# Kernel tuning notes

Hardware: AMD Instinct MI355X
Metric: run time of the kernel (lower is better)

## Reference

```python
import jax, jax.numpy as jnp
import numpy as np

NALGOS = 64
NTASKS = 256
T = 4096  # len(lx)


def setup_inputs() -> dict:
    key = jax.random.key(0)
    ks = jax.random.split(key, 6)
    return {
        "lx": jax.random.randint(ks[0], (T,), 0, NTASKS),
        # task_matrix ~ U(-1, 1), as in the torch init
        "task_matrix": jax.random.uniform(ks[1], (NTASKS, NTASKS), jnp.float32) * 2.0 - 1.0,
        # task difficulty ~ U(0, 1); keep away from 0 to avoid division blowup
        "task_difficulty": jax.random.uniform(ks[2], (NTASKS,), jnp.float32, 0.05, 1.0),
        "alg_efficiency": 0.5 + 0.02 * jax.random.normal(ks[3], (NALGOS,), jnp.float32),
        "alg_memory_horizon": 0.5 + 0.1 * jax.random.normal(ks[4], (NALGOS,), jnp.float32),
        "alg_experience_boost": 0.5 + 0.02 * jax.random.normal(ks[5], (NALGOS,), jnp.float32),
    }


def reference(lx, task_matrix, task_difficulty, alg_efficiency,
              alg_memory_horizon, alg_experience_boost):
    # Faithful translation of IdealLearner.performance.
    # Original triple loop reads result[algo,task2,ind] and sig[algo,task,ind]
    # (previous timestep only) and writes index ind+1, so each timestep is
    # vectorizable over (algo, task2); only the time axis is a true recurrence.
    A = alg_efficiency.shape[0]
    N = task_matrix.shape[0]
    eff = alg_efficiency[:, None]        # (A,1)
    mem = alg_memory_horizon[:, None]    # (A,1)
    boost = alg_experience_boost[:, None]  # (A,1)
    diff = task_difficulty[None, :]      # (1,N) ; task_difficulty_scale == 1

    def step(carry, task):
        res_prev, sig_prev = carry              # each (A, N)
        tm = task_matrix[task][None, :]         # (1, N) row for current task
        sp = sig_prev[:, task][:, None]         # (A, 1) prior perf on current task
        res = res_prev * mem + tm * eff + tm * sp * boost
        sig = 2.0 * jax.nn.sigmoid(res / diff) - 1.0
        return (res, sig), sig

    z = jnp.zeros((A, N), task_matrix.dtype)
    _, ys = jax.lax.scan(step, (z, z), lx)      # ys: (T, A, N)
    # prepend the zero initial state -> (A, N, T+1), matching the torch output
    return jnp.concatenate([z[:, :, None], jnp.transpose(ys, (1, 2, 0))], axis=-1)
```

## Files before the change

### kernel.cpp

```cpp
#include <hip/hip_runtime.h>
#include <hip/hip_bf16.h>

#define NALGOS 64
#define NTASKS 256
#define TSTEPS 4096
#define CHUNK  256
#define NCHUNK (TSTEPS / CHUNK)
#define SUB    64
#define TP     257
#define LOG2E  1.44269504f

__global__ __launch_bounds__(64) void driver_kernel(
    const int* __restrict__ lx, const float* __restrict__ tmat,
    const float* __restrict__ diff, const float* __restrict__ eff_v,
    const float* __restrict__ mem_v, const float* __restrict__ boost_v,
    float* __restrict__ g_arr, float* __restrict__ ckpt) {
  __shared__ int    lx_s[TSTEPS + 16];
  __shared__ float  c_s[NTASKS];
  __shared__ float4 ctab[TSTEPS + 8];

  const int a = blockIdx.x;
  const int l = threadIdx.x;
  const float eff   = eff_v[a];
  const float mem   = mem_v[a];
  const float boost = boost_v[a];
  const float e0 = eff - boost;
  const float b2 = 2.0f * boost;

#pragma unroll 8
  for (int k = 0; k < TSTEPS / 64; ++k) lx_s[k * 64 + l] = lx[k * 64 + l];
  if (l < 16) lx_s[TSTEPS + l] = 0;
#pragma unroll
  for (int k = 0; k < NTASKS / 64; ++k) {
    float dk = diff[k * 64 + l];
    c_s[k * 64 + l] = -LOG2E / dk;
  }
  __syncthreads();

#pragma unroll 4
  for (int k = 0; k < TSTEPS / 64; ++k) {
    int i  = k * 64 + l;
    int t0 = lx_s[i];
    int t1 = lx_s[i + 1];
    float q  = tmat[t0 * NTASKS + t1];
    float cp = c_s[t1];
    float4 e;
    e.x = cp;
    e.y = b2 * cp * q;
    e.z = e0 * cp * q;
    e.w = __int_as_float(lx_s[i + 2] | (lx_s[i + 8] << 16));
    ctab[i] = e;
  }
  if (l < 8) ctab[TSTEPS + l] = make_float4(0.f, 0.f, 0.f, __int_as_float(0));
  __syncthreads();

  const float4* rows = (const float4*)tmat;
  float* gout = g_arr + (size_t)a * TSTEPS;
  float* ck   = ckpt  + (size_t)a * NCHUNK * NTASKS;

  float r0 = 0.f, r1 = 0.f, r2 = 0.f, r3 = 0.f;
  float u = 2.0f;
  float keep_g = 0.f;

  float4 ctr[4];
  float4 tmr[8];
#pragma unroll
  for (int k = 0; k < 4; ++k) ctr[k] = ctab[k];
#pragma unroll
  for (int k = 0; k < 8; ++k) tmr[k] = rows[lx_s[k] * 64 + l];
  float A = ctr[0].z;

  for (int grp = 0; grp < TSTEPS / 64; ++grp) {
#pragma unroll 1
    for (int k32 = 0; k32 < 2; ++k32) {
      const float4* cb = ctab + grp * 64 + k32 * 32;
      const int kb = k32 * 32;
#pragma unroll
      for (int kk = 0; kk < 32; ++kk) {
        const int k = kb + kk;
        const float4 ct  = ctr[k & 3];
        const float4 ctn = ctr[(k + 1) & 3];
        const float4 tm  = tmr[k & 7];

        float w   = __builtin_amdgcn_rcpf(u);
        float gt  = fmaf(b2, w, e0);
        float arg = fmaf(ct.y, w, A);
        float ev  = __builtin_amdgcn_exp2f(arg);
        u = 1.0f + ev;

        keep_g = (k == l) ? gt : keep_g;

        r0 = fmaf(r0, mem, tm.x * gt);
        r1 = fmaf(r1, mem, tm.y * gt);
        r2 = fmaf(r2, mem, tm.z * gt);
        r3 = fmaf(r3, mem, tm.w * gt);

        const int sw   = __builtin_amdgcn_readfirstlane(__float_as_int(ct.w));
        const int j2   = sw & 0xff;
        const int lane = j2 >> 2;
        float h01  = (j2 & 1) ? r1 : r0;
        float h23  = (j2 & 1) ? r3 : r2;
        float hsel = (j2 & 2) ? h23 : h01;
        float bro = __uint_as_float(
            __builtin_amdgcn_readlane(__float_as_uint(hsel), lane));
        float p = mem * bro;
        A = fmaf(ctn.x, p, ctn.z);

        ctr[k & 3] = cb[kk + 4];
        const int nrow = (sw >> 16) & 0xff;
        tmr[k & 7] = rows[nrow * 64 + l];
      }
    }
    gout[grp * 64 + l] = keep_g;
    if ((grp & 3) == 3 && grp != 63) {
      float4 s; s.x = r0; s.y = r1; s.z = r2; s.w = r3;
      ((float4*)(ck + ((grp + 1) >> 2) * NTASKS))[l] = s;
    }
  }
}

__global__ __launch_bounds__(256) void expand_kernel(
    const int* __restrict__ lx, const float* __restrict__ tmat,
    const float* __restrict__ diff, const float* __restrict__ mem_v,
    const float* __restrict__ g_arr, const float* __restrict__ ckpt,
    float* __restrict__ out) {
  __shared__ float tile[SUB * TP];
  __shared__ int   lx_c[CHUNK];
  __shared__ float g_c[CHUNK];

  const int id = blockIdx.x;
  const int c  = (id >> 3) & 15;
  const int a  = (id & 7) + 8 * (id >> 7);
  const int n  = threadIdx.x;

  const float mem = mem_v[a];
  const float cn  = -LOG2E / diff[n];
  float res = (c == 0) ? 0.f : ckpt[((size_t)a * NCHUNK + c) * NTASKS + n];

  const int t0 = c * CHUNK;
  lx_c[n] = lx[t0 + n];
  g_c[n]  = g_arr[(size_t)a * TSTEPS + t0 + n];
  __syncthreads();

  if (c == 0) out[((size_t)a * NTASKS + n) * (TSTEPS + 1)] = 0.f;

  const int tq   = threadIdx.x & 15;
  const int rloc = threadIdx.x >> 4;

  for (int tb = 0; tb < CHUNK; tb += SUB) {
#pragma unroll 8
    for (int ts = 0; ts < SUB; ++ts) {
      int   task = lx_c[tb + ts];
      float g    = g_c[tb + ts];
      float tm   = tmat[task * NTASKS + n];
      res = fmaf(res, mem, tm * g);
      float w = __builtin_amdgcn_rcpf(
          1.0f + __builtin_amdgcn_exp2f(cn * res));
      tile[ts * TP + n] = fmaf(2.0f, w, -1.0f);
    }
    __syncthreads();
    for (int rr = 0; rr < NTASKS; rr += 16) {
      const int row = rr + rloc;
      float v0 = tile[(4 * tq + 0) * TP + row];
      float v1 = tile[(4 * tq + 1) * TP + row];
      float v2 = tile[(4 * tq + 2) * TP + row];
      float v3 = tile[(4 * tq + 3) * TP + row];
      float4 v = make_float4(v0, v1, v2, v3);
      float* dst = &out[((size_t)a * NTASKS + row) * (TSTEPS + 1) +
                        t0 + tb + 4 * tq + 1];
      __builtin_memcpy(dst, &v, 16);
    }
    __syncthreads();
  }
}

extern "C" void kernel_launch(void* const* d_in, const int* in_sizes, int n_in,
                              void* d_out, int out_size, void* d_ws, size_t ws_size,
                              hipStream_t stream) {
  const int*   lx    = (const int*)d_in[0];
  const float* tmat  = (const float*)d_in[1];
  const float* diff  = (const float*)d_in[2];
  const float* eff   = (const float*)d_in[3];
  const float* mem   = (const float*)d_in[4];
  const float* boost = (const float*)d_in[5];
  float* out = (float*)d_out;

  float* g_arr = (float*)d_ws;
  float* ckpt  = g_arr + (size_t)NALGOS * TSTEPS;

  driver_kernel<<<NALGOS, 64, 0, stream>>>(lx, tmat, diff, eff, mem, boost,
                                           g_arr, ckpt);
  expand_kernel<<<dim3(NCHUNK * NALGOS), 256, 0, stream>>>(
      lx, tmat, diff, mem, g_arr, ckpt, out);
}
```

Measured before the change: 611.5 us.

## Unroll serial recurrence two steps to shorten dependency chain; shrink expand sub-tile

```diff
diff --git a/kernel.cpp b/kernel.cpp
--- a/kernel.cpp
+++ b/kernel.cpp
@@ -6,7 +6,7 @@
 #define TSTEPS 4096
 #define CHUNK  256
 #define NCHUNK (TSTEPS / CHUNK)
-#define SUB    64
+#define SUB    32
 #define TP     257
 #define LOG2E  1.44269504f
 
@@ -18,6 +18,7 @@
   __shared__ int    lx_s[TSTEPS + 16];
   __shared__ float  c_s[NTASKS];
   __shared__ float4 ctab[TSTEPS + 8];
+  __shared__ int    itab[TSTEPS + 8];
 
   const int a = blockIdx.x;
   const int l = threadIdx.x;
@@ -26,6 +27,7 @@
   const float boost = boost_v[a];
   const float e0 = eff - boost;
   const float b2 = 2.0f * boost;
+  const float m2 = mem * mem;
 
 #pragma unroll 8
   for (int k = 0; k < TSTEPS / 64; ++k) lx_s[k * 64 + l] = lx[k * 64 + l];
@@ -40,18 +42,23 @@
 #pragma unroll 4
   for (int k = 0; k < TSTEPS / 64; ++k) {
     int i  = k * 64 + l;
-    int t0 = lx_s[i];
     int t1 = lx_s[i + 1];
-    float q  = tmat[t0 * NTASKS + t1];
+    float q  = tmat[lx_s[i] * NTASKS + t1];
+    float q2 = (i >= 1) ? tmat[lx_s[i - 1] * NTASKS + t1]
+                        : 0.f;
     float cp = c_s[t1];
     float4 e;
-    e.x = cp;
-    e.y = b2 * cp * q;
-    e.z = e0 * cp * q;
-    e.w = __int_as_float(lx_s[i + 2] | (lx_s[i + 8] << 16));
+    e.x = b2 * cp * q;
+    e.y = b2 * cp * mem * q2;
+    e.z = e0 * cp * (q + mem * q2);
+    e.w = cp * m2;
     ctab[i] = e;
-  }
-  if (l < 8) ctab[TSTEPS + l] = make_float4(0.f, 0.f, 0.f, __int_as_float(0));
+    itab[i] = lx_s[i + 3] | (lx_s[i + 8] << 16);
+  }
+  if (l < 8) {
+    ctab[TSTEPS + l] = make_float4(0.f, 0.f, 0.f, 0.f);
+    itab[TSTEPS + l] = 0;
+  }
   __syncthreads();
 
   const float4* rows = (const float4*)tmat;
@@ -63,30 +70,37 @@
   float keep_g = 0.f;
 
   float4 ctr[4];
+  int    itr[4];
   float4 tmr[8];
 #pragma unroll
-  for (int k = 0; k < 4; ++k) ctr[k] = ctab[k];
+  for (int k = 0; k < 4; ++k) { ctr[k] = ctab[k]; itr[k] = itab[k]; }
 #pragma unroll
   for (int k = 0; k < 8; ++k) tmr[k] = rows[lx_s[k] * 64 + l];
-  float A = ctr[0].z;
+  float A    = ctr[0].z;
+  float base = ctr[1].z;
 
   for (int grp = 0; grp < TSTEPS / 64; ++grp) {
 #pragma unroll 1
     for (int k32 = 0; k32 < 2; ++k32) {
       const float4* cb = ctab + grp * 64 + k32 * 32;
+      const int*    ib = itab + grp * 64 + k32 * 32;
       const int kb = k32 * 32;
 #pragma unroll
       for (int kk = 0; kk < 32; ++kk) {
         const int k = kb + kk;
-        const float4 ct  = ctr[k & 3];
-        const float4 ctn = ctr[(k + 1) & 3];
+        const float4 ct0 = ctr[k & 3];
+        const float4 ct1 = ctr[(k + 1) & 3];
+        const float4 ct2 = ctr[(k + 2) & 3];
         const float4 tm  = tmr[k & 7];
+        const int    it  = itr[k & 3];
 
         float w   = __builtin_amdgcn_rcpf(u);
-        float gt  = fmaf(b2, w, e0);
-        float arg = fmaf(ct.y, w, A);
+        float arg = fmaf(ct0.x, w, A);
         float ev  = __builtin_amdgcn_exp2f(arg);
         u = 1.0f + ev;
+
+        float gt = fmaf(b2, w, e0);
+        A = fmaf(ct1.y, w, base);
 
         keep_g = (k == l) ? gt : keep_g;
 
@@ -95,18 +109,18 @@
         r2 = fmaf(r2, mem, tm.z * gt);
         r3 = fmaf(r3, mem, tm.w * gt);
 
-        const int sw   = __builtin_amdgcn_readfirstlane(__float_as_int(ct.w));
-        const int j2   = sw & 0xff;
-        const int lane = j2 >> 2;
-        float h01  = (j2 & 1) ? r1 : r0;
-        float h23  = (j2 & 1) ? r3 : r2;
-        float hsel = (j2 & 2) ? h23 : h01;
+        const int sw   = __builtin_amdgcn_readfirstlane(it);
+        const int j    = sw & 0xff;
+        const int lane = j >> 2;
+        float h01  = (j & 1) ? r1 : r0;
+        float h23  = (j & 1) ? r3 : r2;
+        float hsel = (j & 2) ? h23 : h01;
         float bro = __uint_as_float(
             __builtin_amdgcn_readlane(__float_as_uint(hsel), lane));
-        float p = mem * bro;
-        A = fmaf(ctn.x, p, ctn.z);
+        base = fmaf(ct2.w, bro, ct2.z);
 
         ctr[k & 3] = cb[kk + 4];
+        itr[k & 3] = ib[kk + 4];
         const int nrow = (sw >> 16) & 0xff;
         tmr[k & 7] = rows[nrow * 64 + l];
       }
@@ -144,8 +158,8 @@
 
   if (c == 0) out[((size_t)a * NTASKS + n) * (TSTEPS + 1)] = 0.f;
 
-  const int tq   = threadIdx.x & 15;
-  const int rloc = threadIdx.x >> 4;
+  const int tq   = threadIdx.x & 7;
+  const int rloc = threadIdx.x >> 3;
 
   for (int tb = 0; tb < CHUNK; tb += SUB) {
 #pragma unroll 8
@@ -159,7 +173,7 @@
       tile[ts * TP + n] = fmaf(2.0f, w, -1.0f);
     }
     __syncthreads();
-    for (int rr = 0; rr < NTASKS; rr += 16) {
+    for (int rr = 0; rr < NTASKS; rr += 32) {
       const int row = rr + rloc;
       float v0 = tile[(4 * tq + 0) * TP + row];
       float v1 = tile[(4 * tq + 1) * TP + row];
```

New measurement: 655.7 us. 7.2% more time.

## Lookahead-two recurrence in driver to take readlane broadcast off critical path

Applied to the files above, without the earlier changes.

```diff
diff --git a/kernel.cpp b/kernel.cpp
--- a/kernel.cpp
+++ b/kernel.cpp
@@ -17,7 +17,8 @@
     float* __restrict__ g_arr, float* __restrict__ ckpt) {
   __shared__ int    lx_s[TSTEPS + 16];
   __shared__ float  c_s[NTASKS];
-  __shared__ float4 ctab[TSTEPS + 8];
+  __shared__ float4 ptab[TSTEPS + 64];
+  __shared__ int    itab[TSTEPS + 64];
 
   const int a = blockIdx.x;
   const int l = threadIdx.x;
@@ -26,6 +27,7 @@
   const float boost = boost_v[a];
   const float e0 = eff - boost;
   const float b2 = 2.0f * boost;
+  const float m2 = mem * mem;
 
 #pragma unroll 8
   for (int k = 0; k < TSTEPS / 64; ++k) lx_s[k * 64 + l] = lx[k * 64 + l];
@@ -37,21 +39,30 @@
   }
   __syncthreads();
 
-#pragma unroll 4
+#pragma unroll 2
   for (int k = 0; k < TSTEPS / 64; ++k) {
     int i  = k * 64 + l;
     int t0 = lx_s[i];
     int t1 = lx_s[i + 1];
-    float q  = tmat[t0 * NTASKS + t1];
-    float cp = c_s[t1];
+    int t2 = lx_s[i + 2];
+    int t3 = lx_s[i + 3];
+    float q_i   = tmat[t0 * NTASKS + t1];
+    float q2_i1 = tmat[t0 * NTASKS + t2];
+    float q_i2  = tmat[t2 * NTASKS + t3];
+    float q2_i2 = tmat[t1 * NTASKS + t3];
+    float cp1 = c_s[t1];
+    float cp2 = c_s[t2];
+    float cp3 = c_s[t3];
     float4 e;
-    e.x = cp;
-    e.y = b2 * cp * q;
-    e.z = e0 * cp * q;
-    e.w = __int_as_float(lx_s[i + 2] | (lx_s[i + 8] << 16));
-    ctab[i] = e;
-  }
-  if (l < 8) ctab[TSTEPS + l] = make_float4(0.f, 0.f, 0.f, __int_as_float(0));
+    e.x = b2 * cp1 * q_i;
+    e.y = b2 * cp2 * mem * q2_i1;
+    e.z = e0 * cp3 * (q_i2 + mem * q2_i2);
+    e.w = cp3 * m2;
+    ptab[i] = e;
+    itab[i] = t3 | (lx_s[i + 8] << 16);
+  }
+  ptab[TSTEPS + l] = make_float4(0.f, 0.f, 0.f, 0.f);
+  itab[TSTEPS + l] = 0;
   __syncthreads();
 
   const float4* rows = (const float4*)tmat;
@@ -62,55 +73,69 @@
   float u = 2.0f;
   float keep_g = 0.f;
 
-  float4 ctr[4];
+  {
+    int l0 = lx_s[0], l1 = lx_s[1], l2 = lx_s[2];
+    float A0 = e0 * c_s[l1] * tmat[l0 * NTASKS + l1];
+    float B1 = e0 * c_s[l2] *
+               (tmat[l1 * NTASKS + l2] + mem * tmat[l0 * NTASKS + l2]);
+    r0 = r0;
+    (void)A0; (void)B1;
+  }
+  int l0 = lx_s[0], l1 = lx_s[1], l2 = lx_s[2];
+  float A    = e0 * c_s[l1] * tmat[l0 * NTASKS + l1];
+  float base = e0 * c_s[l2] *
+               (tmat[l1 * NTASKS + l2] + mem * tmat[l0 * NTASKS + l2]);
+
+  float4 pc = ptab[l];
+  int    ic = itab[l];
   float4 tmr[8];
 #pragma unroll
-  for (int k = 0; k < 4; ++k) ctr[k] = ctab[k];
+  for (int k = 0; k < 8; ++k) tmr[k] = rows[lx_s[k] * 64 + l];
+
+  for (int grp = 0; grp < TSTEPS / 64; ++grp) {
+    const float4 pn  = ptab[grp * 64 + 64 + l];
+    const int    in_ = itab[grp * 64 + 64 + l];
 #pragma unroll
-  for (int k = 0; k < 8; ++k) tmr[k] = rows[lx_s[k] * 64 + l];
-  float A = ctr[0].z;
-
-  for (int grp = 0; grp < TSTEPS / 64; ++grp) {
-#pragma unroll 1
-    for (int k32 = 0; k32 < 2; ++k32) {
-      const float4* cb = ctab + grp * 64 + k32 * 32;
-      const int kb = k32 * 32;
-#pragma unroll
-      for (int kk = 0; kk < 32; ++kk) {
-        const int k = kb + kk;
-        const float4 ct  = ctr[k & 3];
-        const float4 ctn = ctr[(k + 1) & 3];
-        const float4 tm  = tmr[k & 7];
-
-        float w   = __builtin_amdgcn_rcpf(u);
-        float gt  = fmaf(b2, w, e0);
-        float arg = fmaf(ct.y, w, A);
-        float ev  = __builtin_amdgcn_exp2f(arg);
-        u = 1.0f + ev;
-
-        keep_g = (k == l) ? gt : keep_g;
-
-        r0 = fmaf(r0, mem, tm.x * gt);
-        r1 = fmaf(r1, mem, tm.y * gt);
-        r2 = fmaf(r2, mem, tm.z * gt);
-        r3 = fmaf(r3, mem, tm.w * gt);
-
-        const int sw   = __builtin_amdgcn_readfirstlane(__float_as_int(ct.w));
-        const int j2   = sw & 0xff;
-        const int lane = j2 >> 2;
-        float h01  = (j2 & 1) ? r1 : r0;
-        float h23  = (j2 & 1) ? r3 : r2;
-        float hsel = (j2 & 2) ? h23 : h01;
-        float bro = __uint_as_float(
-            __builtin_amdgcn_readlane(__float_as_uint(hsel), lane));
-        float p = mem * bro;
-        A = fmaf(ctn.x, p, ctn.z);
-
-        ctr[k & 3] = cb[kk + 4];
-        const int nrow = (sw >> 16) & 0xff;
-        tmr[k & 7] = rows[nrow * 64 + l];
-      }
-    }
+    for (int kk = 0; kk < 64; ++kk) {
+      const float X = __uint_as_float(
+          __builtin_amdgcn_readlane(__float_as_uint(pc.x), kk));
+      const float Y = __uint_as_float(
+          __builtin_amdgcn_readlane(__float_as_uint(pc.y), kk));
+      const float Z = __uint_as_float(
+          __builtin_amdgcn_readlane(__float_as_uint(pc.z), kk));
+      const float E = __uint_as_float(
+          __builtin_amdgcn_readlane(__float_as_uint(pc.w), kk));
+      const int  it = __builtin_amdgcn_readlane(ic, kk);
+      const float4 tm = tmr[kk & 7];
+
+      float w   = __builtin_amdgcn_rcpf(u);
+      float arg = fmaf(X, w, A);
+      float ev  = __builtin_amdgcn_exp2f(arg);
+      u = 1.0f + ev;
+
+      float gt = fmaf(b2, w, e0);
+      A = fmaf(Y, w, base);
+
+      keep_g = (kk == l) ? gt : keep_g;
+
+      r0 = fmaf(r0, mem, tm.x * gt);
+      r1 = fmaf(r1, mem, tm.y * gt);
+      r2 = fmaf(r2, mem, tm.z * gt);
+      r3 = fmaf(r3, mem, tm.w * gt);
+
+      const int j    = it & 0xff;
+      const int lane = j >> 2;
+      float h01  = (j & 1) ? r1 : r0;
+      float h23  = (j & 1) ? r3 : r2;
+      float hsel = (j & 2) ? h23 : h01;
+      float bro = __uint_as_float(
+          __builtin_amdgcn_readlane(__float_as_uint(hsel), lane));
+      base = fmaf(E, bro, Z);
+
+      const int nrow = (it >> 16) & 0xff;
+      tmr[kk & 7] = rows[nrow * 64 + l];
+    }
+    pc = pn; ic = in_;
     gout[grp * 64 + l] = keep_g;
     if ((grp & 3) == 3 && grp != 63) {
       float4 s; s.x = r0; s.y = r1; s.z = r2; s.w = r3;
```

Result: slower. 672.0 us (+9.9%).
